# Kernel optimization log

Hardware: AMD Instinct MI355X
Metric: run time of the kernel (lower is better)

The kernel has to match this reference:

```python
import jax, jax.numpy as jnp
import numpy as np

B, N = 1, 4096
D_IN, D_OUT, H = 256, 256, 8
HD = D_OUT // H
NEG = -9e15


def _xavier(key, shape):
    lim = np.sqrt(6.0 / (shape[0] + shape[1])).astype(np.float32)
    return jax.random.uniform(key, shape, jnp.float32, -lim, lim)


def setup_inputs() -> dict:
    key = jax.random.key(0)
    ks = jax.random.split(key, 8)
    x = jax.random.normal(ks[0], (B, N, D_IN), jnp.float32)
    adj = (jax.random.uniform(ks[1], (B, N, N)) < 0.05).astype(jnp.float32)
    idx = jnp.arange(N)
    adj = adj.at[:, idx, idx].set(1.0)
    Wq = _xavier(ks[2], (D_IN, D_OUT)); bq = jnp.zeros((D_OUT,), jnp.float32)
    Wk = _xavier(ks[3], (D_IN, D_OUT)); bk = jnp.zeros((D_OUT,), jnp.float32)
    Wv = _xavier(ks[4], (D_IN, D_OUT)); bv = jnp.zeros((D_OUT,), jnp.float32)
    Wo = _xavier(ks[5], (D_OUT, D_OUT)); bo = jnp.zeros((D_OUT,), jnp.float32)
    return dict(x=x, adj=adj, Wq=Wq, bq=bq, Wk=Wk, bk=bk, Wv=Wv, bv=bv, Wo=Wo, bo=bo)


def reference(x, adj, Wq, bq, Wk, bk, Wv, bv, Wo, bo):
    b, n, _ = x.shape
    def split_heads(t):  # [B,N,D_OUT] -> [B,H,N,HD]
        return t.reshape(b, n, H, HD).transpose(0, 2, 1, 3)
    q = split_heads(x @ Wq + bq)
    k = split_heads(x @ Wk + bk)
    v = split_heads(x @ Wv + bv)
    scores = jnp.einsum('bhqd,bhkd->bhqk', q, k) / np.float32(np.sqrt(HD))
    scores = jnp.where(adj[:, None, :, :] > 0, scores, jnp.float32(NEG))
    attn = jax.nn.softmax(scores, axis=-1)
    # dropout is identity in eval mode (training=False)
    out = jnp.einsum('bhqk,bhkd->bhqd', attn, v)
    out = out.transpose(0, 2, 1, 3).reshape(b, n, D_OUT)
    return out @ Wo + bo
```

## Files before the change

kernel.cpp:

```cpp
#include <hip/hip_runtime.h>
#include <hip/hip_bf16.h>
#include <stdint.h>

#define NTOK 4096
#define DIM  256
#define NH   8
#define HD   32
#define MAXNNZ 512

typedef __attribute__((ext_vector_type(8))) short short8;
typedef __attribute__((ext_vector_type(4))) float float4v;
typedef unsigned short u16;
typedef unsigned int u32;

__device__ __forceinline__ float bf2f(u16 u) {
    union { u32 u; float f; } c; c.u = ((u32)u) << 16; return c.f;
}
__device__ __forceinline__ u16 f2bf(float f) {
    union { float f; u32 u; } c; c.f = f;
    u32 u = c.u;
    u = u + 0x7FFFu + ((u >> 16) & 1u);
    return (u16)(u >> 16);
}
__device__ __forceinline__ float blo(u32 c) {
    union { u32 u; float f; } x; x.u = c << 16; return x.f;
}
__device__ __forceinline__ float bhi(u32 c) {
    union { u32 u; float f; } x; x.u = c & 0xFFFF0000u; return x.f;
}

__global__ void x_to_bf16(const float* __restrict__ x, u16* __restrict__ xb) {
    int i = (blockIdx.x * blockDim.x + threadIdx.x) * 4;
    float4 v = *(const float4*)(x + i);
    ushort4 o;
    o.x = f2bf(v.x); o.y = f2bf(v.y); o.z = f2bf(v.z); o.w = f2bf(v.w);
    *(ushort4*)(xb + i) = o;
}

__global__ void transpose_w(const float* __restrict__ Wq, const float* __restrict__ Wk,
                            const float* __restrict__ Wv, const float* __restrict__ Wo,
                            u16* __restrict__ WT) {
    const float* srcs[4] = {Wq, Wk, Wv, Wo};
    const float* W = srcs[blockIdx.y];
    int o = blockIdx.x, i = threadIdx.x;
    WT[blockIdx.y * 65536 + o * 256 + i] = f2bf(W[i * 256 + o]);
}

__global__ __launch_bounds__(256) void adj_to_list(const float* __restrict__ adj,
                                                   u16* __restrict__ NL,
                                                   u32* __restrict__ NC) {
    __shared__ u32 cnt;
    int row = blockIdx.x, t = threadIdx.x;
    if (t == 0) cnt = 0;
    __syncthreads();
    const float4* rp = (const float4*)(adj + (size_t)row * NTOK);
    u16* lbase = NL + (size_t)row * MAXNNZ;
#pragma unroll
    for (int i = 0; i < 4; ++i) {
        float4 v = rp[i * 256 + t];
        u32 m = 0;
        if (v.x != 0.f) m |= 1u;
        if (v.y != 0.f) m |= 2u;
        if (v.z != 0.f) m |= 4u;
        if (v.w != 0.f) m |= 8u;
        if (m) {
            int p = __popc(m);
            u32 base = atomicAdd(&cnt, (u32)p);
            int col0 = (i * 256 + t) * 4;
            while (m) {
                int j = __builtin_ctz(m);
                m &= m - 1;
                if (base < MAXNNZ) lbase[base] = (u16)(col0 + j);
                ++base;
            }
        }
    }
    __syncthreads();
    if (t == 0) NC[row] = (cnt < MAXNNZ) ? cnt : MAXNNZ;
}

__global__ __launch_bounds__(64) void qkv_gemm(
    const u16* __restrict__ xb,
    const u16* __restrict__ WT,
    const float* __restrict__ bq, const float* __restrict__ bk, const float* __restrict__ bv,
    u16* __restrict__ Q, u16* __restrict__ K, u16* __restrict__ V) {
    int lane = threadIdx.x, quad = lane >> 4, l16 = lane & 15;
    int mtile = blockIdx.x, ntile = blockIdx.y, mat = blockIdx.z;
    const float* bias = (mat == 0) ? bq : (mat == 1) ? bk : bv;
    const u16* arow = xb + (size_t)(mtile * 16 + l16) * DIM + quad * 8;
    const u16* brow = WT + (size_t)mat * 65536 + (size_t)(ntile * 16 + l16) * DIM + quad * 8;
    float4v acc = {0.f, 0.f, 0.f, 0.f};
#pragma unroll
    for (int k0 = 0; k0 < DIM; k0 += 32) {
        short8 af = *(const short8*)(arow + k0);
        short8 bf = *(const short8*)(brow + k0);
        acc = __builtin_amdgcn_mfma_f32_16x16x32_bf16(af, bf, acc, 0, 0, 0);
    }
    int n = ntile * 16 + l16;
    float bb = bias[n];
    const float sc = (mat == 0) ? 0.25503635559913516f : 1.0f;
    u16* dst = (mat == 0) ? Q : (mat == 1) ? K : V;
#pragma unroll
    for (int r = 0; r < 4; ++r) {
        int m = mtile * 16 + quad * 4 + r;
        dst[(size_t)m * DIM + n] = f2bf((acc[r] + bb) * sc);
    }
}

#define UNPK8(C, B) do { \
    q[B+0]=blo(C.x); q[B+1]=bhi(C.x); q[B+2]=blo(C.y); q[B+3]=bhi(C.y); \
    q[B+4]=blo(C.z); q[B+5]=bhi(C.z); q[B+6]=blo(C.w); q[B+7]=bhi(C.w); } while(0)

#define DOT8(C, A, B) do { \
    A = fmaf(blo(C.x), q[B+0], A); A = fmaf(bhi(C.x), q[B+1], A); \
    A = fmaf(blo(C.y), q[B+2], A); A = fmaf(bhi(C.y), q[B+3], A); \
    A = fmaf(blo(C.z), q[B+4], A); A = fmaf(bhi(C.z), q[B+5], A); \
    A = fmaf(blo(C.w), q[B+6], A); A = fmaf(bhi(C.w), q[B+7], A); } while(0)

#define PV8(C, B) do { \
    O[B+0]=fmaf(e, blo(C.x), O[B+0]); O[B+1]=fmaf(e, bhi(C.x), O[B+1]); \
    O[B+2]=fmaf(e, blo(C.y), O[B+2]); O[B+3]=fmaf(e, bhi(C.y), O[B+3]); \
    O[B+4]=fmaf(e, blo(C.z), O[B+4]); O[B+5]=fmaf(e, bhi(C.z), O[B+5]); \
    O[B+6]=fmaf(e, blo(C.w), O[B+6]); O[B+7]=fmaf(e, bhi(C.w), O[B+7]); } while(0)

__global__ __launch_bounds__(256, 4) void sparse_attn(
    const u16* __restrict__ Q, const u16* __restrict__ K, const u16* __restrict__ V,
    const u16* __restrict__ NL, const u32* __restrict__ NC,
    u16* __restrict__ AO) {
    int row = blockIdx.x * 4 + (threadIdx.x >> 6);
    int lane = threadIdx.x & 63;
    int h = lane & 7;
    int s = lane >> 3;

    const uint4* qp = (const uint4*)(Q + (size_t)row * DIM + h * HD);
    uint4 qq0 = qp[0], qq1 = qp[1], qq2 = qp[2], qq3 = qp[3];
    float q[32];
    UNPK8(qq0, 0); UNPK8(qq1, 8); UNPK8(qq2, 16); UNPK8(qq3, 24);

    float O[32];
#pragma unroll
    for (int i = 0; i < 32; ++i) O[i] = 0.f;
    float lsum = 0.f;

    int nnz = (int)NC[row];
    const u16* lst = NL + (size_t)row * MAXNNZ;
    const u16* Kh = K + h * HD;
    const u16* Vh = V + h * HD;

    int jj = (s < nnz) ? s : (nnz - 1);
    int idx = lst[jj];
    for (int j0 = 0; j0 < nnz; j0 += 8) {
        bool valid = (j0 + s) < nnz;
        const uint4* kp = (const uint4*)(Kh + (size_t)idx * DIM);
        const uint4* vp = (const uint4*)(Vh + (size_t)idx * DIM);
        uint4 k0 = kp[0], k1 = kp[1], k2 = kp[2], k3 = kp[3];
        uint4 v0 = vp[0], v1 = vp[1], v2 = vp[2], v3 = vp[3];
        int jn = j0 + 8 + s;
        jn = (jn < nnz) ? jn : (nnz - 1);
        idx = lst[jn];

        float a0 = 0.f, a1 = 0.f, a2 = 0.f, a3 = 0.f;
        DOT8(k0, a0, 0); DOT8(k1, a1, 8); DOT8(k2, a2, 16); DOT8(k3, a3, 24);
        float sd = (a0 + a1) + (a2 + a3);
        float e = __builtin_amdgcn_exp2f(sd);
        e = valid ? e : 0.f;
        lsum += e;
        PV8(v0, 0); PV8(v1, 8); PV8(v2, 16); PV8(v3, 24);
    }

#pragma unroll
    for (int i = 0; i < 32; ++i) O[i] += __shfl_xor(O[i], 8, 64);
#pragma unroll
    for (int i = 0; i < 32; ++i) O[i] += __shfl_xor(O[i], 16, 64);
#pragma unroll
    for (int i = 0; i < 32; ++i) O[i] += __shfl_xor(O[i], 32, 64);
    lsum += __shfl_xor(lsum, 8, 64);
    lsum += __shfl_xor(lsum, 16, 64);
    lsum += __shfl_xor(lsum, 32, 64);

    if (s == 0) {
        float inv = 1.0f / lsum;
        u32 w[16];
#pragma unroll
        for (int i = 0; i < 16; ++i) {
            u32 lo16 = (u32)f2bf(O[2 * i] * inv);
            u32 hi16 = (u32)f2bf(O[2 * i + 1] * inv);
            w[i] = lo16 | (hi16 << 16);
        }
        uint4* dst = (uint4*)(AO + (size_t)row * DIM + h * HD);
        dst[0] = make_uint4(w[0], w[1], w[2], w[3]);
        dst[1] = make_uint4(w[4], w[5], w[6], w[7]);
        dst[2] = make_uint4(w[8], w[9], w[10], w[11]);
        dst[3] = make_uint4(w[12], w[13], w[14], w[15]);
    }
}

__global__ __launch_bounds__(64) void out_gemm(
    const u16* __restrict__ AO, const u16* __restrict__ WTo, const float* __restrict__ bo,
    float* __restrict__ out) {
    int lane = threadIdx.x, quad = lane >> 4, l16 = lane & 15;
    int mtile = blockIdx.x, ntile = blockIdx.y;
    const u16* arow = AO + (size_t)(mtile * 16 + l16) * DIM + quad * 8;
    const u16* brow = WTo + (size_t)(ntile * 16 + l16) * DIM + quad * 8;
    float4v acc = {0.f, 0.f, 0.f, 0.f};
#pragma unroll
    for (int k0 = 0; k0 < DIM; k0 += 32) {
        short8 af = *(const short8*)(arow + k0);
        short8 bf = *(const short8*)(brow + k0);
        acc = __builtin_amdgcn_mfma_f32_16x16x32_bf16(af, bf, acc, 0, 0, 0);
    }
    int n = ntile * 16 + l16;
    float bb = bo[n];
#pragma unroll
    for (int r = 0; r < 4; ++r)
        out[(size_t)(mtile * 16 + quad * 4 + r) * DIM + n] = acc[r] + bb;
}

extern "C" void kernel_launch(void* const* d_in, const int* in_sizes, int n_in,
                              void* d_out, int out_size, void* d_ws, size_t ws_size,
                              hipStream_t stream) {
    const float* x   = (const float*)d_in[0];
    const float* adj = (const float*)d_in[1];
    const float* Wq  = (const float*)d_in[2];
    const float* bq  = (const float*)d_in[3];
    const float* Wk  = (const float*)d_in[4];
    const float* bk  = (const float*)d_in[5];
    const float* Wv  = (const float*)d_in[6];
    const float* bv  = (const float*)d_in[7];
    const float* Wo  = (const float*)d_in[8];
    const float* bo  = (const float*)d_in[9];

    char* ws = (char*)d_ws;
    const size_t MB = 1u << 20;
    u16* Q   = (u16*)(ws);
    u16* K   = (u16*)(ws + 2 * MB);
    u16* V   = (u16*)(ws + 4 * MB);
    u16* AO  = (u16*)(ws + 6 * MB);
    u16* WT  = (u16*)(ws + 8 * MB);
    u16* XB  = (u16*)(ws + 8 * MB + 512 * 1024);
    u16* NL  = (u16*)(ws + 11 * MB);
    u32* NC  = (u32*)(ws + 15 * MB);

    x_to_bf16<<<dim3(1024), 256, 0, stream>>>(x, XB);
    transpose_w<<<dim3(256, 4), 256, 0, stream>>>(Wq, Wk, Wv, Wo, WT);
    adj_to_list<<<dim3(4096), 256, 0, stream>>>(adj, NL, NC);
    qkv_gemm<<<dim3(256, 16, 3), 64, 0, stream>>>(XB, WT, bq, bk, bv, Q, K, V);
    sparse_attn<<<dim3(1024), 256, 0, stream>>>(Q, K, V, NL, NC, AO);
    out_gemm<<<dim3(256, 16), 64, 0, stream>>>(AO, WT + 3 * 65536, bo, (float*)d_out);
}
```

Before: 212.0 us.

## Remap sparse attention lanes to split head dims and process neighbor pairs

The thread mapping in sparse_attn changes from each lane owning a whole head (32 dims) across 8 neighbor slots to each lane owning 8 dims of a row, with two half-wavefronts handling alternating neighbors. Dot products are reduced across 4 lanes with shuffles, and neighbor indices are loaded as packed 32-bit pairs with prefetch. This gives coalesced 512-byte contiguous K/V row reads per neighbor and fewer registers per lane, cutting the final 3-stage reduction to one. The cost is more shuffles per neighbor and less neighbor parallelism per wave.

```diff
diff --git a/kernel.cpp b/kernel.cpp
--- a/kernel.cpp
+++ b/kernel.cpp
@@ -107,91 +107,86 @@
     }
 }
 
-#define UNPK8(C, B) do { \
-    q[B+0]=blo(C.x); q[B+1]=bhi(C.x); q[B+2]=blo(C.y); q[B+3]=bhi(C.y); \
-    q[B+4]=blo(C.z); q[B+5]=bhi(C.z); q[B+6]=blo(C.w); q[B+7]=bhi(C.w); } while(0)
-
-#define DOT8(C, A, B) do { \
-    A = fmaf(blo(C.x), q[B+0], A); A = fmaf(bhi(C.x), q[B+1], A); \
-    A = fmaf(blo(C.y), q[B+2], A); A = fmaf(bhi(C.y), q[B+3], A); \
-    A = fmaf(blo(C.z), q[B+4], A); A = fmaf(bhi(C.z), q[B+5], A); \
-    A = fmaf(blo(C.w), q[B+6], A); A = fmaf(bhi(C.w), q[B+7], A); } while(0)
-
-#define PV8(C, B) do { \
-    O[B+0]=fmaf(e, blo(C.x), O[B+0]); O[B+1]=fmaf(e, bhi(C.x), O[B+1]); \
-    O[B+2]=fmaf(e, blo(C.y), O[B+2]); O[B+3]=fmaf(e, bhi(C.y), O[B+3]); \
-    O[B+4]=fmaf(e, blo(C.z), O[B+4]); O[B+5]=fmaf(e, bhi(C.z), O[B+5]); \
-    O[B+6]=fmaf(e, blo(C.w), O[B+6]); O[B+7]=fmaf(e, bhi(C.w), O[B+7]); } while(0)
-
 __global__ __launch_bounds__(256, 4) void sparse_attn(
     const u16* __restrict__ Q, const u16* __restrict__ K, const u16* __restrict__ V,
     const u16* __restrict__ NL, const u32* __restrict__ NC,
     u16* __restrict__ AO) {
     int row = blockIdx.x * 4 + (threadIdx.x >> 6);
     int lane = threadIdx.x & 63;
-    int h = lane & 7;
-    int s = lane >> 3;
-
-    const uint4* qp = (const uint4*)(Q + (size_t)row * DIM + h * HD);
-    uint4 qq0 = qp[0], qq1 = qp[1], qq2 = qp[2], qq3 = qp[3];
-    float q[32];
-    UNPK8(qq0, 0); UNPK8(qq1, 8); UNPK8(qq2, 16); UNPK8(qq3, 24);
-
-    float O[32];
-#pragma unroll
-    for (int i = 0; i < 32; ++i) O[i] = 0.f;
+    int p = lane >> 5;
+    int t = lane & 31;
+
+    uint4 qq = *(const uint4*)(Q + (size_t)row * DIM + t * 8);
+    float q0 = blo(qq.x), q1 = bhi(qq.x), q2 = blo(qq.y), q3 = bhi(qq.y);
+    float q4 = blo(qq.z), q5 = bhi(qq.z), q6 = blo(qq.w), q7 = bhi(qq.w);
+
+    float O[8];
+#pragma unroll
+    for (int i = 0; i < 8; ++i) O[i] = 0.f;
     float lsum = 0.f;
 
     int nnz = (int)NC[row];
     const u16* lst = NL + (size_t)row * MAXNNZ;
-    const u16* Kh = K + h * HD;
-    const u16* Vh = V + h * HD;
-
-    int jj = (s < nnz) ? s : (nnz - 1);
-    int idx = lst[jj];
-    for (int j0 = 0; j0 < nnz; j0 += 8) {
-        bool valid = (j0 + s) < nnz;
-        const uint4* kp = (const uint4*)(Kh + (size_t)idx * DIM);
-        const uint4* vp = (const uint4*)(Vh + (size_t)idx * DIM);
-        uint4 k0 = kp[0], k1 = kp[1], k2 = kp[2], k3 = kp[3];
-        uint4 v0 = vp[0], v1 = vp[1], v2 = vp[2], v3 = vp[3];
-        int jn = j0 + 8 + s;
-        jn = (jn < nnz) ? jn : (nnz - 1);
-        idx = lst[jn];
-
-        float a0 = 0.f, a1 = 0.f, a2 = 0.f, a3 = 0.f;
-        DOT8(k0, a0, 0); DOT8(k1, a1, 8); DOT8(k2, a2, 16); DOT8(k3, a3, 24);
-        float sd = (a0 + a1) + (a2 + a3);
-        float e = __builtin_amdgcn_exp2f(sd);
-        e = valid ? e : 0.f;
-        lsum += e;
-        PV8(v0, 0); PV8(v1, 8); PV8(v2, 16); PV8(v3, 24);
-    }
-
-#pragma unroll
-    for (int i = 0; i < 32; ++i) O[i] += __shfl_xor(O[i], 8, 64);
-#pragma unroll
-    for (int i = 0; i < 32; ++i) O[i] += __shfl_xor(O[i], 16, 64);
-#pragma unroll
-    for (int i = 0; i < 32; ++i) O[i] += __shfl_xor(O[i], 32, 64);
-    lsum += __shfl_xor(lsum, 8, 64);
-    lsum += __shfl_xor(lsum, 16, 64);
+    const u16* Kt = K + t * 8;
+    const u16* Vt = V + t * 8;
+
+#define PAIR_BODY(kk, vv, e_valid)                                               \
+    {                                                                            \
+        float a = 0.f, b = 0.f;                                                  \
+        a = fmaf(blo(kk.x), q0, a); b = fmaf(bhi(kk.x), q1, b);                  \
+        a = fmaf(blo(kk.y), q2, a); b = fmaf(bhi(kk.y), q3, b);                  \
+        a = fmaf(blo(kk.z), q4, a); b = fmaf(bhi(kk.z), q5, b);                  \
+        a = fmaf(blo(kk.w), q6, a); b = fmaf(bhi(kk.w), q7, b);                  \
+        float s = a + b;                                                         \
+        s += __shfl_xor(s, 1, 64);                                               \
+        s += __shfl_xor(s, 2, 64);      \
+        float e = __builtin_amdgcn_exp2f(s);                                     \
+        e = (e_valid) ? e : 0.f;                                                 \
+        lsum += e;                                                               \
+        O[0] = fmaf(e, blo(vv.x), O[0]); O[1] = fmaf(e, bhi(vv.x), O[1]);        \
+        O[2] = fmaf(e, blo(vv.y), O[2]); O[3] = fmaf(e, bhi(vv.y), O[3]);        \
+        O[4] = fmaf(e, blo(vv.z), O[4]); O[5] = fmaf(e, bhi(vv.z), O[5]);        \
+        O[6] = fmaf(e, blo(vv.w), O[6]); O[7] = fmaf(e, bhi(vv.w), O[7]);        \
+    }
+
+    u32 wA = *(const u32*)(lst);
+    u32 wB = (nnz > 2) ? *(const u32*)(lst + 2) : wA;
+    for (int i2 = 0; i2 < nnz; i2 += 4) {
+        bool vA = (i2 + p) < nnz;
+        bool vB = (i2 + 2 + p) < nnz;
+        int lo = (int)(wA & 0xFFFFu);
+        int iA = p ? (int)(wA >> 16) : lo;
+        int iB = p ? (int)(wB >> 16) : (int)(wB & 0xFFFFu);
+        if (!vA) iA = lo;
+        if (!vB) iB = lo;
+
+        int in0 = i2 + 4, in2 = i2 + 6;
+        u32 wAn = *(const u32*)(lst + ((in0 < nnz) ? in0 : 0));
+        u32 wBn = *(const u32*)(lst + ((in2 < nnz) ? in2 : 0));
+
+        uint4 kA = *(const uint4*)(Kt + (size_t)iA * DIM);
+        uint4 vAv = *(const uint4*)(Vt + (size_t)iA * DIM);
+        uint4 kB = *(const uint4*)(Kt + (size_t)iB * DIM);
+        uint4 vBv = *(const uint4*)(Vt + (size_t)iB * DIM);
+
+        PAIR_BODY(kA, vAv, vA)
+        PAIR_BODY(kB, vBv, vB)
+
+        wA = wAn; wB = wBn;
+    }
+#undef PAIR_BODY
+
+#pragma unroll
+    for (int i = 0; i < 8; ++i) O[i] += __shfl_xor(O[i], 32, 64);
     lsum += __shfl_xor(lsum, 32, 64);
 
-    if (s == 0) {
+    if (p == 0) {
         float inv = 1.0f / lsum;
-        u32 w[16];
-#pragma unroll
-        for (int i = 0; i < 16; ++i) {
-            u32 lo16 = (u32)f2bf(O[2 * i] * inv);
-            u32 hi16 = (u32)f2bf(O[2 * i + 1] * inv);
-            w[i] = lo16 | (hi16 << 16);
-        }
-        uint4* dst = (uint4*)(AO + (size_t)row * DIM + h * HD);
-        dst[0] = make_uint4(w[0], w[1], w[2], w[3]);
-        dst[1] = make_uint4(w[4], w[5], w[6], w[7]);
-        dst[2] = make_uint4(w[8], w[9], w[10], w[11]);
-        dst[3] = make_uint4(w[12], w[13], w[14], w[15]);
+        u32 w0 = (u32)f2bf(O[0] * inv) | ((u32)f2bf(O[1] * inv) << 16);
+        u32 w1 = (u32)f2bf(O[2] * inv) | ((u32)f2bf(O[3] * inv) << 16);
+        u32 w2 = (u32)f2bf(O[4] * inv) | ((u32)f2bf(O[5] * inv) << 16);
+        u32 w3 = (u32)f2bf(O[6] * inv) | ((u32)f2bf(O[7] * inv) << 16);
+        *(uint4*)(AO + (size_t)row * DIM + t * 8) = make_uint4(w0, w1, w2, w3);
     }
 }
 
```

Result: faster. 199.9 us (-5.7%).
